# Optimization experiments

Hardware: AMD Instinct MI355X
Metric: run time of the kernel (lower is better)

Reference implementation:

```python
import jax, jax.numpy as jnp
import numpy as np


def setup_inputs() -> dict:
    key = jax.random.key(0)
    k1, k2 = jax.random.split(key)
    B, T, D = 16, 4096, 512
    x = jax.random.normal(k1, (B, T, D), dtype=jnp.float32)
    alpha = jax.random.normal(k2, (1, 1, D), dtype=jnp.float32)  # raw param, pre-sigmoid
    return {"x": x, "alpha": alpha}


def reference(x, alpha):
    # s_0 = x_0 ; s_t = a * x_t + (1 - a) * s_{t-1}, a = sigmoid(alpha)
    a = jax.nn.sigmoid(alpha[0, 0, :])  # (D,)
    one_minus_a = 1.0 - a

    def step(prev, xt):  # prev, xt: (B, D)
        cur = a * xt + one_minus_a * prev
        return cur, cur

    x_t = jnp.swapaxes(x, 0, 1)  # (T, B, D)
    init = x_t[0]
    _, rest = jax.lax.scan(step, init, x_t[1:])  # (T-1, B, D)
    states = jnp.concatenate([x_t[:1], rest], axis=0)  # (T, B, D)
    return jnp.swapaxes(states, 0, 1)  # (B, T, D)
```

## Files before the change

### kernel.cpp

```cpp
#include <hip/hip_runtime.h>
#include <math.h>

#define BB 16
#define TT 4096
#define DD 512
#define D4 128

__device__ __forceinline__ float sigmf(float v) {
    return 1.0f / (1.0f + expf(-v));
}

__global__ __launch_bounds__(256) void es_chunk_ends(
    const float* __restrict__ x, const float* __restrict__ alpha,
    float* __restrict__ ends, int C, int L)
{
    const int c   = blockIdx.x;
    const int tid = threadIdx.x;
    const int b   = (blockIdx.y << 1) + (tid >> 7);
    const int d4  = tid & 127;

    const float4 al = reinterpret_cast<const float4*>(alpha)[d4];
    const float ax = sigmf(al.x), ay = sigmf(al.y), az = sigmf(al.z), aw = sigmf(al.w);
    const float fx = 1.0f - ax, fy = 1.0f - ay, fz = 1.0f - az, fw = 1.0f - aw;

    const float4* xp = reinterpret_cast<const float4*>(x)
                     + ((size_t)b * TT + (size_t)c * L) * D4 + d4;

    float4 s;
    if (c == 0) {
        s = xp[0];
    } else {
        s.x = s.y = s.z = s.w = 0.0f;
    }

    #pragma unroll 8
    for (int i = 0; i < L; ++i) {
        const float4 v = xp[(size_t)i * D4];
        s.x = fmaf(ax, v.x, fx * s.x);
        s.y = fmaf(ay, v.y, fy * s.y);
        s.z = fmaf(az, v.z, fz * s.z);
        s.w = fmaf(aw, v.w, fw * s.w);
    }

    reinterpret_cast<float4*>(ends)[((size_t)b * C + c) * D4 + d4] = s;
}

__global__ __launch_bounds__(256) void es_carry_scan(
    float* __restrict__ ends, const float* __restrict__ alpha, int C, int L)
{
    const int g  = blockIdx.x * 256 + threadIdx.x;
    const int b  = g >> 7;
    const int d4 = g & 127;

    const float4 al = reinterpret_cast<const float4*>(alpha)[d4];
    const float ax = sigmf(al.x), ay = sigmf(al.y), az = sigmf(al.z), aw = sigmf(al.w);
    float4 fL;
    fL.x = powf(1.0f - ax, (float)L);
    fL.y = powf(1.0f - ay, (float)L);
    fL.z = powf(1.0f - az, (float)L);
    fL.w = powf(1.0f - aw, (float)L);

    float4* e = reinterpret_cast<float4*>(ends) + (size_t)b * C * D4 + d4;

    float4 S = e[0];
    int c = 1;
    for (; c + 8 <= C; c += 8) {
        float4 v[8];
        #pragma unroll
        for (int j = 0; j < 8; ++j) v[j] = e[(size_t)(c + j) * D4];
        #pragma unroll
        for (int j = 0; j < 8; ++j) {
            S.x = fmaf(fL.x, S.x, v[j].x);
            S.y = fmaf(fL.y, S.y, v[j].y);
            S.z = fmaf(fL.z, S.z, v[j].z);
            S.w = fmaf(fL.w, S.w, v[j].w);
            e[(size_t)(c + j) * D4] = S;
        }
    }
    for (; c < C; ++c) {
        const float4 v = e[(size_t)c * D4];
        S.x = fmaf(fL.x, S.x, v.x);
        S.y = fmaf(fL.y, S.y, v.y);
        S.z = fmaf(fL.z, S.z, v.z);
        S.w = fmaf(fL.w, S.w, v.w);
        e[(size_t)c * D4] = S;
    }
}

__global__ __launch_bounds__(256) void es_final(
    const float* __restrict__ x, const float* __restrict__ alpha,
    const float* __restrict__ finals, float* __restrict__ out, int C, int L)
{
    const int c   = blockIdx.x;
    const int tid = threadIdx.x;
    const int b   = (blockIdx.y << 1) + (tid >> 7);
    const int d4  = tid & 127;

    const float4 al = reinterpret_cast<const float4*>(alpha)[d4];
    const float ax = sigmf(al.x), ay = sigmf(al.y), az = sigmf(al.z), aw = sigmf(al.w);
    const float fx = 1.0f - ax, fy = 1.0f - ay, fz = 1.0f - az, fw = 1.0f - aw;

    const size_t base = ((size_t)b * TT + (size_t)c * L) * D4 + d4;
    const float4* xp = reinterpret_cast<const float4*>(x) + base;
    float4*       op = reinterpret_cast<float4*>(out) + base;

    float4 s;
    if (c == 0) {
        s = xp[0];
    } else {
        s = reinterpret_cast<const float4*>(finals)[((size_t)b * C + (c - 1)) * D4 + d4];
    }

    #pragma unroll 8
    for (int i = 0; i < L; ++i) {
        const float4 v = xp[(size_t)i * D4];
        s.x = fmaf(ax, v.x, fx * s.x);
        s.y = fmaf(ay, v.y, fy * s.y);
        s.z = fmaf(az, v.z, fz * s.z);
        s.w = fmaf(aw, v.w, fw * s.w);
        op[(size_t)i * D4] = s;
    }
}

__global__ __launch_bounds__(256) void es_serial(
    const float* __restrict__ x, const float* __restrict__ alpha,
    float* __restrict__ out)
{
    const int g  = blockIdx.x * 256 + threadIdx.x;
    const int b  = g >> 7;
    const int d4 = g & 127;

    const float4 al = reinterpret_cast<const float4*>(alpha)[d4];
    const float ax = sigmf(al.x), ay = sigmf(al.y), az = sigmf(al.z), aw = sigmf(al.w);
    const float fx = 1.0f - ax, fy = 1.0f - ay, fz = 1.0f - az, fw = 1.0f - aw;

    const float4* xp = reinterpret_cast<const float4*>(x) + (size_t)b * TT * D4 + d4;
    float4*       op = reinterpret_cast<float4*>(out) + (size_t)b * TT * D4 + d4;

    float4 s = xp[0];
    #pragma unroll 4
    for (int t = 0; t < TT; ++t) {
        const float4 v = xp[(size_t)t * D4];
        s.x = fmaf(ax, v.x, fx * s.x);
        s.y = fmaf(ay, v.y, fy * s.y);
        s.z = fmaf(az, v.z, fz * s.z);
        s.w = fmaf(aw, v.w, fw * s.w);
        op[(size_t)t * D4] = s;
    }
}

extern "C" void kernel_launch(void* const* d_in, const int* in_sizes, int n_in,
                              void* d_out, int out_size, void* d_ws, size_t ws_size,
                              hipStream_t stream)
{
    const float* x     = (const float*)d_in[0];
    const float* alpha = (const float*)d_in[1];
    float*       out   = (float*)d_out;

    int C = 128;
    while (C > 8 && (size_t)BB * C * DD * sizeof(float) > ws_size) C >>= 1;

    if ((size_t)BB * C * DD * sizeof(float) > ws_size) {
        es_serial<<<dim3(8), 256, 0, stream>>>(x, alpha, out);
        return;
    }

    const int L = TT / C;
    float* ends = (float*)d_ws;

    es_chunk_ends<<<dim3(C, BB / 2), 256, 0, stream>>>(x, alpha, ends, C, L);
    es_carry_scan<<<dim3(8), 256, 0, stream>>>(ends, alpha, C, L);
    es_final<<<dim3(C, BB / 2), 256, 0, stream>>>(x, alpha, ends, out, C, L);
}
```

Before: 269.5 us.

## Fix chunk count at compile time, batch-load chunk inputs, prefetch carries, nontemporal stores

The chunk count becomes a compile-time constant of 256 (chunks of 16 steps), which doubles the grid size. Each thread now issues all of its chunk's loads up front into registers before running the recurrence, so memory latency overlaps instead of sitting on the serial dependency. The carry scan uses a 16-deep rolling register prefetch buffer, and the final pass writes output with nontemporal stores to avoid polluting the cache. The cost is more register pressure, a larger carry array for the scan to walk serially, and the loss of the adaptive chunk fallback when workspace is small.

```diff
diff --git a/kernel.cpp b/kernel.cpp
--- a/kernel.cpp
+++ b/kernel.cpp
@@ -6,47 +6,55 @@
 #define DD 512
 #define D4 128
 
+constexpr int CC = 256;
+constexpr int LL = TT / CC;
+
+typedef float floatx4 __attribute__((ext_vector_type(4)));
+
 __device__ __forceinline__ float sigmf(float v) {
     return 1.0f / (1.0f + expf(-v));
 }
 
 __global__ __launch_bounds__(256) void es_chunk_ends(
     const float* __restrict__ x, const float* __restrict__ alpha,
-    float* __restrict__ ends, int C, int L)
+    float* __restrict__ ends)
 {
     const int c   = blockIdx.x;
     const int tid = threadIdx.x;
     const int b   = (blockIdx.y << 1) + (tid >> 7);
     const int d4  = tid & 127;
 
+    const float4* xp = reinterpret_cast<const float4*>(x)
+                     + ((size_t)b * TT + (size_t)c * LL) * D4 + d4;
+
+    float4 v[LL];
+    #pragma unroll
+    for (int i = 0; i < LL; ++i) v[i] = xp[(size_t)i * D4];
+
     const float4 al = reinterpret_cast<const float4*>(alpha)[d4];
     const float ax = sigmf(al.x), ay = sigmf(al.y), az = sigmf(al.z), aw = sigmf(al.w);
     const float fx = 1.0f - ax, fy = 1.0f - ay, fz = 1.0f - az, fw = 1.0f - aw;
 
-    const float4* xp = reinterpret_cast<const float4*>(x)
-                     + ((size_t)b * TT + (size_t)c * L) * D4 + d4;
-
     float4 s;
     if (c == 0) {
-        s = xp[0];
+        s = v[0];
     } else {
         s.x = s.y = s.z = s.w = 0.0f;
     }
 
-    #pragma unroll 8
-    for (int i = 0; i < L; ++i) {
-        const float4 v = xp[(size_t)i * D4];
-        s.x = fmaf(ax, v.x, fx * s.x);
-        s.y = fmaf(ay, v.y, fy * s.y);
-        s.z = fmaf(az, v.z, fz * s.z);
-        s.w = fmaf(aw, v.w, fw * s.w);
+    #pragma unroll
+    for (int i = 0; i < LL; ++i) {
+        s.x = fmaf(ax, v[i].x, fx * s.x);
+        s.y = fmaf(ay, v[i].y, fy * s.y);
+        s.z = fmaf(az, v[i].z, fz * s.z);
+        s.w = fmaf(aw, v[i].w, fw * s.w);
     }
 
-    reinterpret_cast<float4*>(ends)[((size_t)b * C + c) * D4 + d4] = s;
+    reinterpret_cast<float4*>(ends)[((size_t)b * CC + c) * D4 + d4] = s;
 }
 
 __global__ __launch_bounds__(256) void es_carry_scan(
-    float* __restrict__ ends, const float* __restrict__ alpha, int C, int L)
+    float* __restrict__ ends, const float* __restrict__ alpha)
 {
     const int g  = blockIdx.x * 256 + threadIdx.x;
     const int b  = g >> 7;
@@ -55,30 +63,36 @@
     const float4 al = reinterpret_cast<const float4*>(alpha)[d4];
     const float ax = sigmf(al.x), ay = sigmf(al.y), az = sigmf(al.z), aw = sigmf(al.w);
     float4 fL;
-    fL.x = powf(1.0f - ax, (float)L);
-    fL.y = powf(1.0f - ay, (float)L);
-    fL.z = powf(1.0f - az, (float)L);
-    fL.w = powf(1.0f - aw, (float)L);
+    fL.x = powf(1.0f - ax, (float)LL);
+    fL.y = powf(1.0f - ay, (float)LL);
+    fL.z = powf(1.0f - az, (float)LL);
+    fL.w = powf(1.0f - aw, (float)LL);
 
-    float4* e = reinterpret_cast<float4*>(ends) + (size_t)b * C * D4 + d4;
+    float4* e = reinterpret_cast<float4*>(ends) + (size_t)b * CC * D4 + d4;
+
+    constexpr int P = 16;
+    float4 buf[P];
+    #pragma unroll
+    for (int j = 0; j < P; ++j) buf[j] = e[(size_t)(1 + j) * D4];
 
     float4 S = e[0];
     int c = 1;
-    for (; c + 8 <= C; c += 8) {
-        float4 v[8];
+    while (c + P <= CC) {
         #pragma unroll
-        for (int j = 0; j < 8; ++j) v[j] = e[(size_t)(c + j) * D4];
-        #pragma unroll
-        for (int j = 0; j < 8; ++j) {
-            S.x = fmaf(fL.x, S.x, v[j].x);
-            S.y = fmaf(fL.y, S.y, v[j].y);
-            S.z = fmaf(fL.z, S.z, v[j].z);
-            S.w = fmaf(fL.w, S.w, v[j].w);
-            e[(size_t)(c + j) * D4] = S;
+        for (int j = 0; j < P; ++j) {
+            const float4 v = buf[j];
+            const int pf = c + P;
+            if (pf < CC) buf[j] = e[(size_t)pf * D4];
+            S.x = fmaf(fL.x, S.x, v.x);
+            S.y = fmaf(fL.y, S.y, v.y);
+            S.z = fmaf(fL.z, S.z, v.z);
+            S.w = fmaf(fL.w, S.w, v.w);
+            e[(size_t)c * D4] = S;
+            ++c;
         }
     }
-    for (; c < C; ++c) {
-        const float4 v = e[(size_t)c * D4];
+    for (int j = 0; c < CC; ++c, ++j) {
+        const float4 v = buf[j];
         S.x = fmaf(fL.x, S.x, v.x);
         S.y = fmaf(fL.y, S.y, v.y);
         S.z = fmaf(fL.z, S.z, v.z);
@@ -89,36 +103,40 @@
 
 __global__ __launch_bounds__(256) void es_final(
     const float* __restrict__ x, const float* __restrict__ alpha,
-    const float* __restrict__ finals, float* __restrict__ out, int C, int L)
+    const float* __restrict__ carries, float* __restrict__ out)
 {
     const int c   = blockIdx.x;
     const int tid = threadIdx.x;
     const int b   = (blockIdx.y << 1) + (tid >> 7);
     const int d4  = tid & 127;
 
+    float4 s;
+    if (c != 0) {
+        s = reinterpret_cast<const float4*>(carries)[((size_t)b * CC + (c - 1)) * D4 + d4];
+    }
+
+    const size_t base = ((size_t)b * TT + (size_t)c * LL) * D4 + d4;
+    const float4* xp = reinterpret_cast<const float4*>(x) + base;
+    floatx4*      op = reinterpret_cast<floatx4*>(out) + base;
+
+    float4 v[LL];
+    #pragma unroll
+    for (int i = 0; i < LL; ++i) v[i] = xp[(size_t)i * D4];
+
     const float4 al = reinterpret_cast<const float4*>(alpha)[d4];
     const float ax = sigmf(al.x), ay = sigmf(al.y), az = sigmf(al.z), aw = sigmf(al.w);
     const float fx = 1.0f - ax, fy = 1.0f - ay, fz = 1.0f - az, fw = 1.0f - aw;
 
-    const size_t base = ((size_t)b * TT + (size_t)c * L) * D4 + d4;
-    const float4* xp = reinterpret_cast<const float4*>(x) + base;
-    float4*       op = reinterpret_cast<float4*>(out) + base;
+    if (c == 0) s = v[0];
 
-    float4 s;
-    if (c == 0) {
-        s = xp[0];
-    } else {
-        s = reinterpret_cast<const float4*>(finals)[((size_t)b * C + (c - 1)) * D4 + d4];
-    }
-
-    #pragma unroll 8
-    for (int i = 0; i < L; ++i) {
-        const float4 v = xp[(size_t)i * D4];
-        s.x = fmaf(ax, v.x, fx * s.x);
-        s.y = fmaf(ay, v.y, fy * s.y);
-        s.z = fmaf(az, v.z, fz * s.z);
-        s.w = fmaf(aw, v.w, fw * s.w);
-        op[(size_t)i * D4] = s;
+    #pragma unroll
+    for (int i = 0; i < LL; ++i) {
+        s.x = fmaf(ax, v[i].x, fx * s.x);
+        s.y = fmaf(ay, v[i].y, fy * s.y);
+        s.z = fmaf(az, v[i].z, fz * s.z);
+        s.w = fmaf(aw, v[i].w, fw * s.w);
+        floatx4 sv = { s.x, s.y, s.z, s.w };
+        __builtin_nontemporal_store(sv, op + (size_t)i * D4);
     }
 }
 
@@ -157,18 +175,14 @@
     const float* alpha = (const float*)d_in[1];
     float*       out   = (float*)d_out;
 
-    int C = 128;
-    while (C > 8 && (size_t)BB * C * DD * sizeof(float) > ws_size) C >>= 1;
-
-    if ((size_t)BB * C * DD * sizeof(float) > ws_size) {
+    const size_t need = (size_t)BB * CC * DD * sizeof(float);
+    if (ws_size < need) {
         es_serial<<<dim3(8), 256, 0, stream>>>(x, alpha, out);
         return;
     }
 
-    const int L = TT / C;
     float* ends = (float*)d_ws;
-
-    es_chunk_ends<<<dim3(C, BB / 2), 256, 0, stream>>>(x, alpha, ends, C, L);
-    es_carry_scan<<<dim3(8), 256, 0, stream>>>(ends, alpha, C, L);
-    es_final<<<dim3(C, BB / 2), 256, 0, stream>>>(x, alpha, ends, out, C, L);
+    es_chunk_ends<<<dim3(CC, BB / 2), 256, 0, stream>>>(x, alpha, ends);
+    es_carry_scan<<<dim3(8), 256, 0, stream>>>(ends, alpha);
+    es_final<<<dim3(CC, BB / 2), 256, 0, stream>>>(x, alpha, ends, out);
 }
```

Result: no change. 270.8 us (+0.5%).
